# Kernel tuning notes

Hardware: AMD Instinct MI355X
Metric: run time of the kernel (lower is better)

Reference implementation:

```python
import jax, jax.numpy as jnp
import numpy as np

N_NODES = 50000
N_EDGES = 300000
HID = 256


def setup_inputs() -> dict:
    key = jax.random.key(0)
    ks = jax.random.split(key, 8)
    s = lambda fan_in: 1.0 / np.sqrt(fan_in)
    return {
        "node_embeddings": jax.random.normal(ks[0], (N_NODES, HID), dtype=jnp.float32),
        "edge_index": jax.random.randint(ks[1], (2, N_EDGES), 0, N_NODES, dtype=jnp.int64),
        "edge_attr": jax.random.normal(ks[2], (N_EDGES, 3), dtype=jnp.float32),
        "W1": jax.random.normal(ks[3], (2 * HID + 3, HID), dtype=jnp.float32) * s(2 * HID + 3),
        "b1": jnp.zeros((HID,), dtype=jnp.float32),
        "W2": jax.random.normal(ks[4], (HID, HID // 2), dtype=jnp.float32) * s(HID),
        "b2": jnp.zeros((HID // 2,), dtype=jnp.float32),
        "W3": jax.random.normal(ks[5], (HID // 2, HID // 4), dtype=jnp.float32) * s(HID // 2),
        "b3": jnp.zeros((HID // 4,), dtype=jnp.float32),
        "W4": jax.random.normal(ks[6], (HID // 4, 3), dtype=jnp.float32) * s(HID // 4),
        "b4": jnp.zeros((3,), dtype=jnp.float32),
    }


def reference(node_embeddings, edge_index, edge_attr, W1, b1, W2, b2, W3, b3, W4, b4):
    # Gather source/target node embeddings: [E, H] each
    src = node_embeddings[edge_index[0]]
    dst = node_embeddings[edge_index[1]]
    feats = jnp.concatenate([src, dst, edge_attr], axis=-1)  # [E, 2H+3]
    # edge_encoder: Linear -> ReLU -> (Dropout=identity in eval) -> Linear
    h = jax.nn.relu(feats @ W1 + b1)
    h = h @ W2 + b2  # [E, H//2]
    # classifier: Linear -> ReLU -> Linear
    h = jax.nn.relu(h @ W3 + b3)
    logits = h @ W4 + b4  # [E, 3]
    return logits
```

## Files before the change

kernel.cpp:

```cpp
#include <hip/hip_runtime.h>
#include <hip/hip_bf16.h>
#include <stdint.h>
#include <stddef.h>


#define NN 50000
#define NE 300000
#define KG(kq,g2) ((kq)*2+(g2))

using bf16x8 = __attribute__((ext_vector_type(8))) short;
using f32x16 = __attribute__((ext_vector_type(16))) float;
using f32x4  = __attribute__((ext_vector_type(4))) float;
using f32x2  = __attribute__((ext_vector_type(2))) float;
using u32x4  = __attribute__((ext_vector_type(4))) unsigned int;
using u32x2  = __attribute__((ext_vector_type(2))) unsigned int;

#define OFF_PQ   0ULL
#define SZ_PQ    (50000ULL*512ULL*2ULL)
#define OFF_W1   (OFF_PQ + SZ_PQ)
#define SZ_W1    (512ULL*256ULL*2ULL)
#define OFF_W1C  (OFF_W1 + SZ_W1)
#define SZ_W1C   (3ULL*256ULL*4ULL)
#define OFF_W2   (OFF_W1C + SZ_W1C)
#define SZ_W2    (128ULL*256ULL*2ULL)
#define OFF_W3   (OFF_W2 + SZ_W2)
#define SZ_W3    (64ULL*128ULL*2ULL)
#define OFF_W4   (OFF_W3 + SZ_W3)
#define SZ_W4    (16ULL*64ULL*2ULL)
#define OFF_FLAG (OFF_W4 + SZ_W4)
#define WS_NEED  (OFF_FLAG + 16ULL)

__device__ __forceinline__ unsigned short f2bf(float x){
  unsigned u = __float_as_uint(x);
  unsigned r = 0x7FFFu + ((u >> 16) & 1u);
  return (unsigned short)((u + r) >> 16);
}
__device__ __forceinline__ unsigned cvtpk(float lo, float hi){
  unsigned r;
  asm("v_cvt_pk_bf16_f32 %0, %1, %2" : "=v"(r) : "v"(lo), "v"(hi));
  return r;
}
__device__ __forceinline__ f32x2 unpk(unsigned w){
  f32x2 r;
  r[0] = __uint_as_float(w << 16);
  r[1] = __uint_as_float(w & 0xFFFF0000u);
  return r;
}
__device__ __forceinline__ f32x16 mfma32(bf16x8 a, bf16x8 b, f32x16 c){
  return __builtin_amdgcn_mfma_f32_32x32x16_bf16(a, b, c, 0, 0, 0);
}
__device__ __forceinline__ f32x4 mfma16(bf16x8 a, bf16x8 b, f32x4 c){
  return __builtin_amdgcn_mfma_f32_16x16x32_bf16(a, b, c, 0, 0, 0);
}
__device__ __forceinline__ f32x16 zero16(){
  f32x16 v;
#pragma unroll
  for (int i = 0; i < 16; ++i) v[i] = 0.f;
  return v;
}

__global__ void prep_pack(const float* __restrict__ W1, const float* __restrict__ W2,
                          const float* __restrict__ W3, const float* __restrict__ W4,
                          const int* __restrict__ ei32, char* __restrict__ ws)
{
  int i = blockIdx.x * 256 + threadIdx.x;
  unsigned short* w1i = (unsigned short*)(ws + OFF_W1);
  unsigned short* w2i = (unsigned short*)(ws + OFF_W2);
  unsigned short* w3i = (unsigned short*)(ws + OFF_W3);
  unsigned short* w4i = (unsigned short*)(ws + OFF_W4);

  if (i < 131072){
    int j = i & 7, out = (i >> 3) & 511, kg = i >> 12;
    int k = (kg >> 1)*16 + (kg & 1)*8 + j;
    float v = (out < 256) ? W1[(size_t)k*256 + out]
                          : W1[(size_t)(256 + k)*256 + (out - 256)];
    w1i[i] = f2bf(v);
  } else if (i < 131072 + 32768){
    int i2 = i - 131072;
    int j = i2 & 7, out = (i2 >> 3) & 127, sg = i2 >> 10;
    int k = (sg >> 2)*32 + (sg & 3)*8 + j;
    w2i[i2] = f2bf(W2[(size_t)k*128 + out]);
  } else if (i < 131072 + 32768 + 8192){
    int i3 = i - 131072 - 32768;
    int j = i3 & 7, out = (i3 >> 3) & 63, sg = i3 >> 9;
    int k = (sg >> 2)*32 + (sg & 3)*8 + j;
    w3i[i3] = f2bf(W3[(size_t)k*64 + out]);
  } else if (i < 131072 + 32768 + 8192 + 1024){
    int i4 = i - 131072 - 32768 - 8192;
    int j = i4 & 7, out = (i4 >> 3) & 15, sg = i4 >> 7;
    int k = (sg >> 2)*32 + (sg & 3)*8 + j;
    w4i[i4] = (out < 3) ? f2bf(W4[(size_t)k*3 + out]) : (unsigned short)0;
  }
  if (i < 768){
    float* w1c = (float*)(ws + OFF_W1C);
    w1c[i] = W1[(size_t)(512 + i/256)*256 + (i & 255)];
  }
  if (i == 0){
    int f = 1;
    for (int t = 1; t < 64; t += 2) if (ei32[t] != 0) { f = 0; break; }
    *(int*)(ws + OFF_FLAG) = f;
  }
}

__global__ __launch_bounds__(512, 4) void gemm1(const float* __restrict__ emb,
                                                const float* __restrict__ b1,
                                                char* __restrict__ ws)
{
  __shared__ __align__(16) unsigned short embL[32*64*8];

  const int tid = threadIdx.x;
  const int wv = tid >> 6, l = tid & 63, ln = l & 31, g2 = l >> 5;
  const int bid = blockIdx.x;
  const int nb = (bid >> 1) * 64;
  const int oh = bid & 1;
  const int ob = oh*256 + wv*32;
  const unsigned short* w1L = (const unsigned short*)(ws + OFF_W1);
  unsigned short* PQ = (unsigned short*)(ws + OFF_PQ);

  bf16x8 aw[16];
#pragma unroll
  for (int kq = 0; kq < 16; ++kq)
    aw[kq] = *(const bf16x8*)(w1L + ((size_t)KG(kq,g2)*512 + ob + ln)*8);

#pragma unroll
  for (int it = 0; it < 8; ++it){
    int u = it*512 + tid;
    int kg = u >> 7, node = (u >> 1) & 63, half = u & 1;
    int n = nb + node; if (n >= NN) n = NN - 1;
    int k = (kg >> 1)*16 + (kg & 1)*8 + half*4;
    f32x4 e = *(const f32x4*)(emb + (size_t)n*256 + k);
    u32x2 w; w[0] = cvtpk(e[0], e[1]); w[1] = cvtpk(e[2], e[3]);
    *(u32x2*)(embL + (size_t)kg*512 + node*8 + half*4) = w;
  }
  __syncthreads();

  f32x16 acc0 = zero16(), acc1 = zero16();
#pragma unroll
  for (int kq = 0; kq < 16; ++kq){
    bf16x8 b0  = *(const bf16x8*)(embL + ((size_t)KG(kq,g2)*64 +      ln)*8);
    bf16x8 b1v = *(const bf16x8*)(embL + ((size_t)KG(kq,g2)*64 + 32 + ln)*8);
    acc0 = mfma32(aw[kq], b0,  acc0);
    acc1 = mfma32(aw[kq], b1v, acc1);
  }

#pragma unroll
  for (int bg = 0; bg < 2; ++bg){
    int n = nb + bg*32 + ln;
    if (n < NN){
#pragma unroll
      for (int rr = 0; rr < 4; ++rr){
        int o = ob + rr*8 + g2*4;
        f32x4 bv = {0.f,0.f,0.f,0.f};
        if (oh == 0) bv = *(const f32x4*)(b1 + o);
        unsigned d0, d1;
        if (bg == 0){
          d0 = cvtpk(acc0[rr*4+0]+bv[0], acc0[rr*4+1]+bv[1]);
          d1 = cvtpk(acc0[rr*4+2]+bv[2], acc0[rr*4+3]+bv[3]);
        } else {
          d0 = cvtpk(acc1[rr*4+0]+bv[0], acc1[rr*4+1]+bv[1]);
          d1 = cvtpk(acc1[rr*4+2]+bv[2], acc1[rr*4+3]+bv[3]);
        }
        u32x2 st = {d0, d1};
        *(u32x2*)(PQ + (size_t)n*512 + o) = st;
      }
    }
  }
}


#define PAIRX(LO, HI, D) ((D)==0 ? (f32x2){(LO)[0],(LO)[1]} : \
                          (D)==1 ? (f32x2){(LO)[2],(LO)[3]} : \
                          (D)==2 ? (f32x2){(HI)[0],(HI)[1]} : \
                                   (f32x2){(HI)[2],(HI)[3]})

#define L2STEP(S, X)                                                           \
  {                                                                            \
    const int ks_ = (S);                                                       \
    bf16x8 pc = p##X, qc = q##X;                                               \
    int kp = ks_ + 2; if (kp > 7) kp = 7;                                      \
    p##X = *(const bf16x8*)(PQ + (size_t)si*512 + kp*32 + g4*8);               \
    q##X = *(const bf16x8*)(PQ + (size_t)di*512 + 256 + kp*32 + g4*8);         \
    const int kb = ks_*32 + g4*8;                                              \
    f32x4 w0lo = *(const f32x4*)(w1c_lds +   0 + kb);                          \
    f32x4 w0hi = *(const f32x4*)(w1c_lds +   4 + kb);                          \
    f32x4 w1lo = *(const f32x4*)(w1c_lds + 256 + kb);                          \
    f32x4 w1hi = *(const f32x4*)(w1c_lds + 260 + kb);                          \
    f32x4 w2lo = *(const f32x4*)(w1c_lds + 512 + kb);                          \
    f32x4 w2hi = *(const f32x4*)(w1c_lds + 516 + kb);                          \
    u32x4 pu = __builtin_bit_cast(u32x4, pc);                                  \
    u32x4 qu = __builtin_bit_cast(u32x4, qc);                                  \
    f32x2 z2 = {0.f, 0.f};                                                     \
    unsigned bu0, bu1, bu2, bu3;                                               \
    _Pragma("unroll")                                                          \
    for (int d = 0; d < 4; ++d){                                               \
      f32x2 h = unpk(pu[d]) + unpk(qu[d]);                                     \
      h += PAIRX(w0lo, w0hi, d) * at0;                                         \
      h += PAIRX(w1lo, w1hi, d) * at1;                                         \
      h += PAIRX(w2lo, w2hi, d) * at2;                                         \
      h = __builtin_elementwise_max(h, z2);                                    \
      unsigned c = cvtpk(h[0], h[1]);                                          \
      if (d==0) bu0 = c; else if (d==1) bu1 = c; else if (d==2) bu2 = c;       \
      else bu3 = c;                                                            \
    }                                                                          \
    u32x4 buv = {bu0, bu1, bu2, bu3};                                          \
    bf16x8 b = __builtin_bit_cast(bf16x8, buv);                                \
    const char* abase = smem + (size_t)(ks_*4 + g4)*2048 + c16*16;             \
    _Pragma("unroll")                                                          \
    for (int t = 0; t < 8; ++t){                                               \
      bf16x8 af = *(const bf16x8*)(abase + t*256);                             \
      acc2[t] = mfma16(af, b, acc2[t]);                                        \
    }                                                                          \
  }

__global__ __launch_bounds__(512, 4) void fused(const int* __restrict__ eidx,
                                                const float* __restrict__ attr,
                                                const float* __restrict__ b2,
                                                const float* __restrict__ b3,
                                                const float* __restrict__ b4,
                                                const char* __restrict__ ws,
                                                float* __restrict__ out)
{
  __shared__ __align__(16) char smem[68608];
  const int tid = threadIdx.x;
  const int wv = tid >> 6, l = tid & 63, c16 = l & 15, g4 = l >> 4;

  const unsigned short* PQ = (const unsigned short*)(ws + OFF_PQ);
  const float* W1c = (const float*)(ws + OFF_W1C);
  const int flag64 = *(const int*)(ws + OFF_FLAG);
  const float* w1c_lds = (const float*)(smem + 65536);

  {
    const uint4* src = (const uint4*)(ws + OFF_W2);
    uint4* dst = (uint4*)smem;
#pragma unroll
    for (int it = 0; it < 8; ++it) dst[it*512 + tid] = src[it*512 + tid];
    if (tid < 192) ((f32x4*)(smem + 65536))[tid] = ((const f32x4*)W1c)[tid];
  }
  __syncthreads();

  const int eb = blockIdx.x * 128 + wv * 16;
  const int e = eb + c16;
  const bool ev = (e < NE);
  const int ec = ev ? e : 0;
  const int si = flag64 ? eidx[2*(size_t)ec]        : eidx[ec];
  const int di = flag64 ? eidx[2*((size_t)NE + ec)] : eidx[NE + ec];
  const float at0 = ev ? attr[(size_t)ec*3 + 0] : 0.f;
  const float at1 = ev ? attr[(size_t)ec*3 + 1] : 0.f;
  const float at2 = ev ? attr[(size_t)ec*3 + 2] : 0.f;

  f32x4 acc2[8];
#pragma unroll
  for (int t = 0; t < 8; ++t) acc2[t] = (f32x4){0.f,0.f,0.f,0.f};

  bf16x8 pA, qA, pB, qB;
  pA = *(const bf16x8*)(PQ + (size_t)si*512 + g4*8);
  qA = *(const bf16x8*)(PQ + (size_t)di*512 + 256 + g4*8);
  pB = *(const bf16x8*)(PQ + (size_t)si*512 + 32 + g4*8);
  qB = *(const bf16x8*)(PQ + (size_t)di*512 + 256 + 32 + g4*8);

#pragma unroll 1
  for (int sb = 0; sb < 4; ++sb){
    L2STEP(2*sb,     A);
    L2STEP(2*sb + 1, B);
  }

  __syncthreads();

  {
    const uint4* s3 = (const uint4*)(ws + OFF_W3);
    uint4* d3 = (uint4*)(smem + 36864);
    for (int i = tid; i < 1152; i += 512) d3[i] = s3[i];
  }

  unsigned short* hslot = (unsigned short*)(smem + wv*4352);
#pragma unroll
  for (int t = 0; t < 8; ++t){
    f32x4 bv = *(const f32x4*)(b2 + t*16 + g4*4);
    unsigned d0 = cvtpk(acc2[t][0]+bv[0], acc2[t][1]+bv[1]);
    unsigned d1 = cvtpk(acc2[t][2]+bv[2], acc2[t][3]+bv[3]);
    u32x2 st = {d0, d1};
    *(u32x2*)(hslot + (size_t)c16*136 + t*16 + g4*4) = st;
  }
  __syncthreads();

  f32x4 acc3[4];
#pragma unroll
  for (int t = 0; t < 4; ++t) acc3[t] = (f32x4){0.f,0.f,0.f,0.f};
  const char* w3b = smem + 36864;
#pragma unroll
  for (int ks = 0; ks < 4; ++ks){
    bf16x8 bb = *(const bf16x8*)(hslot + (size_t)c16*136 + ks*32 + g4*8);
    const char* ab = w3b + (size_t)(ks*4 + g4)*1024 + c16*16;
#pragma unroll
    for (int t = 0; t < 4; ++t){
      bf16x8 af = *(const bf16x8*)(ab + t*256);
      acc3[t] = mfma16(af, bb, acc3[t]);
    }
  }

#pragma unroll
  for (int t = 0; t < 4; ++t){
    f32x4 bv = *(const f32x4*)(b3 + t*16 + g4*4);
    unsigned d0 = cvtpk(fmaxf(acc3[t][0]+bv[0],0.f), fmaxf(acc3[t][1]+bv[1],0.f));
    unsigned d1 = cvtpk(fmaxf(acc3[t][2]+bv[2],0.f), fmaxf(acc3[t][3]+bv[3],0.f));
    u32x2 st = {d0, d1};
    *(u32x2*)(hslot + (size_t)c16*136 + t*16 + g4*4) = st;
  }

  f32x4 acc4 = {0.f,0.f,0.f,0.f};
  const char* w4b = smem + 53248;
#pragma unroll
  for (int ks = 0; ks < 2; ++ks){
    bf16x8 bb = *(const bf16x8*)(hslot + (size_t)c16*136 + ks*32 + g4*8);
    bf16x8 af = *(const bf16x8*)(w4b + (size_t)(ks*4 + g4)*256 + c16*16);
    acc4 = mfma16(af, bb, acc4);
  }
  if (g4 == 0 && ev){
    out[(size_t)e*3 + 0] = acc4[0] + b4[0];
    out[(size_t)e*3 + 1] = acc4[1] + b4[1];
    out[(size_t)e*3 + 2] = acc4[2] + b4[2];
  }
}

extern "C" void kernel_launch(void* const* d_in, const int* in_sizes, int n_in,
                              void* d_out, int out_size, void* d_ws, size_t ws_size,
                              hipStream_t stream)
{
  const float* emb  = (const float*)d_in[0];
  const int*   eidx = (const int*)  d_in[1];
  const float* attr = (const float*)d_in[2];
  const float* W1   = (const float*)d_in[3];
  const float* b1   = (const float*)d_in[4];
  const float* W2   = (const float*)d_in[5];
  const float* b2   = (const float*)d_in[6];
  const float* W3   = (const float*)d_in[7];
  const float* b3   = (const float*)d_in[8];
  const float* W4   = (const float*)d_in[9];
  const float* b4   = (const float*)d_in[10];
  char* ws = (char*)d_ws;
  float* out = (float*)d_out;

  if (ws_size < WS_NEED) return;

  prep_pack<<<676, 256, 0, stream>>>(W1, W2, W3, W4, eidx, ws);
  gemm1<<<((NN + 63)/64)*2, 512, 0, stream>>>(emb, b1, ws);
  fused<<<(NE + 127)/128, 512, 0, stream>>>(eidx, attr, b2, b3, b4, ws, out);
}
```

Measured before the change: 117.4 us.

## Double per-wave edge and output tiles, deepen PQ gather prefetch with inline asm

gemm1 now has each block compute all 512 outputs for its 64 nodes, so each wave holds two weight tiles and embeddings are loaded and converted once rather than twice. The fused kernel handles 32 edges per wave instead of 16, so each W2 LDS fragment feeds two MFMAs. The PQ gathers are issued three stages ahead with raw global_load asm and explicit vmcnt waits to hide gather latency. W3/W4 are now read straight from global memory instead of being staged in LDS. The cost is higher register pressure, lower launch-bound occupancy (4 to 3 and 2), and fragile hand-managed waitcnt ordering.

After: 148.8 us. 26.8% more time.

```diff
diff --git a/kernel.cpp b/kernel.cpp
--- a/kernel.cpp
+++ b/kernel.cpp
@@ -57,6 +57,9 @@
 #pragma unroll
   for (int i = 0; i < 16; ++i) v[i] = 0.f;
   return v;
+}
+__device__ __forceinline__ void gld16(bf16x8& r, const unsigned short* p){
+  asm volatile("global_load_dwordx4 %0, %1, off" : "=&v"(r) : "v"(p));
 }
 
 __global__ void prep_pack(const float* __restrict__ W1, const float* __restrict__ W2,
@@ -102,7 +105,7 @@
   }
 }
 
-__global__ __launch_bounds__(512, 4) void gemm1(const float* __restrict__ emb,
+__global__ __launch_bounds__(512, 2) void gemm1(const float* __restrict__ emb,
                                                 const float* __restrict__ b1,
                                                 char* __restrict__ ws)
 {
@@ -110,17 +113,18 @@
 
   const int tid = threadIdx.x;
   const int wv = tid >> 6, l = tid & 63, ln = l & 31, g2 = l >> 5;
-  const int bid = blockIdx.x;
-  const int nb = (bid >> 1) * 64;
-  const int oh = bid & 1;
-  const int ob = oh*256 + wv*32;
+  const int nb = blockIdx.x * 64;
+  const int ob = wv * 64;
   const unsigned short* w1L = (const unsigned short*)(ws + OFF_W1);
   unsigned short* PQ = (unsigned short*)(ws + OFF_PQ);
 
-  bf16x8 aw[16];
-#pragma unroll
-  for (int kq = 0; kq < 16; ++kq)
-    aw[kq] = *(const bf16x8*)(w1L + ((size_t)KG(kq,g2)*512 + ob + ln)*8);
+  bf16x8 aw[2][16];
+#pragma unroll
+  for (int kq = 0; kq < 16; ++kq){
+#pragma unroll
+    for (int t2 = 0; t2 < 2; ++t2)
+      aw[t2][kq] = *(const bf16x8*)(w1L + ((size_t)KG(kq,g2)*512 + ob + t2*32 + ln)*8);
+  }
 
 #pragma unroll
   for (int it = 0; it < 8; ++it){
@@ -134,34 +138,35 @@
   }
   __syncthreads();
 
-  f32x16 acc0 = zero16(), acc1 = zero16();
+  f32x16 acc[2][2];
+  acc[0][0] = zero16(); acc[0][1] = zero16();
+  acc[1][0] = zero16(); acc[1][1] = zero16();
 #pragma unroll
   for (int kq = 0; kq < 16; ++kq){
     bf16x8 b0  = *(const bf16x8*)(embL + ((size_t)KG(kq,g2)*64 +      ln)*8);
     bf16x8 b1v = *(const bf16x8*)(embL + ((size_t)KG(kq,g2)*64 + 32 + ln)*8);
-    acc0 = mfma32(aw[kq], b0,  acc0);
-    acc1 = mfma32(aw[kq], b1v, acc1);
-  }
-
-#pragma unroll
-  for (int bg = 0; bg < 2; ++bg){
-    int n = nb + bg*32 + ln;
-    if (n < NN){
-#pragma unroll
-      for (int rr = 0; rr < 4; ++rr){
-        int o = ob + rr*8 + g2*4;
-        f32x4 bv = {0.f,0.f,0.f,0.f};
-        if (oh == 0) bv = *(const f32x4*)(b1 + o);
-        unsigned d0, d1;
-        if (bg == 0){
-          d0 = cvtpk(acc0[rr*4+0]+bv[0], acc0[rr*4+1]+bv[1]);
-          d1 = cvtpk(acc0[rr*4+2]+bv[2], acc0[rr*4+3]+bv[3]);
-        } else {
-          d0 = cvtpk(acc1[rr*4+0]+bv[0], acc1[rr*4+1]+bv[1]);
-          d1 = cvtpk(acc1[rr*4+2]+bv[2], acc1[rr*4+3]+bv[3]);
+    acc[0][0] = mfma32(aw[0][kq], b0,  acc[0][0]);
+    acc[1][0] = mfma32(aw[1][kq], b0,  acc[1][0]);
+    acc[0][1] = mfma32(aw[0][kq], b1v, acc[0][1]);
+    acc[1][1] = mfma32(aw[1][kq], b1v, acc[1][1]);
+  }
+
+#pragma unroll
+  for (int t2 = 0; t2 < 2; ++t2){
+#pragma unroll
+    for (int bg = 0; bg < 2; ++bg){
+      int n = nb + bg*32 + ln;
+      if (n < NN){
+#pragma unroll
+        for (int rr = 0; rr < 4; ++rr){
+          int o = ob + t2*32 + rr*8 + g2*4;
+          f32x4 bv = {0.f,0.f,0.f,0.f};
+          if (ob + t2*32 < 256) bv = *(const f32x4*)(b1 + o);
+          unsigned d0 = cvtpk(acc[t2][bg][rr*4+0]+bv[0], acc[t2][bg][rr*4+1]+bv[1]);
+          unsigned d1 = cvtpk(acc[t2][bg][rr*4+2]+bv[2], acc[t2][bg][rr*4+3]+bv[3]);
+          u32x2 st = {d0, d1};
+          *(u32x2*)(PQ + (size_t)n*512 + o) = st;
         }
-        u32x2 st = {d0, d1};
-        *(u32x2*)(PQ + (size_t)n*512 + o) = st;
       }
     }
   }
@@ -173,46 +178,58 @@
                           (D)==2 ? (f32x2){(HI)[0],(HI)[1]} : \
                                    (f32x2){(HI)[2],(HI)[3]})
 
-#define L2STEP(S, X)                                                           \
+#define H1BUILD(PC, QC, A0, A1, A2, BOUT)                                      \
   {                                                                            \
-    const int ks_ = (S);                                                       \
-    bf16x8 pc = p##X, qc = q##X;                                               \
-    int kp = ks_ + 2; if (kp > 7) kp = 7;                                      \
-    p##X = *(const bf16x8*)(PQ + (size_t)si*512 + kp*32 + g4*8);               \
-    q##X = *(const bf16x8*)(PQ + (size_t)di*512 + 256 + kp*32 + g4*8);         \
-    const int kb = ks_*32 + g4*8;                                              \
+    u32x4 pu = __builtin_bit_cast(u32x4, PC);                                  \
+    u32x4 qu = __builtin_bit_cast(u32x4, QC);                                  \
+    f32x2 z2 = {0.f, 0.f};                                                     \
+    unsigned bu0, bu1, bu2, bu3;                                               \
+    _Pragma("unroll")                                                          \
+    for (int d = 0; d < 4; ++d){                                               \
+      f32x2 h = unpk(pu[d]) + unpk(qu[d]);                                     \
+      h += PAIRX(w0lo, w0hi, d) * (A0);                                        \
+      h += PAIRX(w1lo, w1hi, d) * (A1);                                        \
+      h += PAIRX(w2lo, w2hi, d) * (A2);                                        \
+      h = __builtin_elementwise_max(h, z2);                                    \
+      unsigned c = cvtpk(h[0], h[1]);                                          \
+      if (d==0) bu0 = c; else if (d==1) bu1 = c; else if (d==2) bu2 = c;       \
+      else bu3 = c;                                                            \
+    }                                                                          \
+    u32x4 buv = {bu0, bu1, bu2, bu3};                                          \
+    BOUT = __builtin_bit_cast(bf16x8, buv);                                    \
+  }
+
+#define PQWAIT(N, P0, Q0, P1, Q1) \
+  asm volatile("s_waitcnt vmcnt(" #N ")" : "+v"(P0), "+v"(Q0), "+v"(P1), "+v"(Q1))
+
+#define ISSUE4(P0, Q0, P1, Q1, S)                                              \
+  { gld16(P0, Prow0 + (S)*32); gld16(Q0, Qrow0 + (S)*32);                      \
+    gld16(P1, Prow1 + (S)*32); gld16(Q1, Qrow1 + (S)*32); }
+
+#define L2S(S, VM, P0, Q0, P1, Q1, DO_ISS, IS)                                 \
+  {                                                                            \
+    PQWAIT(VM, P0, Q0, P1, Q1);                                                \
+    const int kb = (S)*32 + g4*8;                                              \
     f32x4 w0lo = *(const f32x4*)(w1c_lds +   0 + kb);                          \
     f32x4 w0hi = *(const f32x4*)(w1c_lds +   4 + kb);                          \
     f32x4 w1lo = *(const f32x4*)(w1c_lds + 256 + kb);                          \
     f32x4 w1hi = *(const f32x4*)(w1c_lds + 260 + kb);                          \
     f32x4 w2lo = *(const f32x4*)(w1c_lds + 512 + kb);                          \
     f32x4 w2hi = *(const f32x4*)(w1c_lds + 516 + kb);                          \
-    u32x4 pu = __builtin_bit_cast(u32x4, pc);                                  \
-    u32x4 qu = __builtin_bit_cast(u32x4, qc);                                  \
-    f32x2 z2 = {0.f, 0.f};                                                     \
-    unsigned bu0, bu1, bu2, bu3;                                               \
-    _Pragma("unroll")                                                          \
-    for (int d = 0; d < 4; ++d){                                               \
-      f32x2 h = unpk(pu[d]) + unpk(qu[d]);                                     \
-      h += PAIRX(w0lo, w0hi, d) * at0;                                         \
-      h += PAIRX(w1lo, w1hi, d) * at1;                                         \
-      h += PAIRX(w2lo, w2hi, d) * at2;                                         \
-      h = __builtin_elementwise_max(h, z2);                                    \
-      unsigned c = cvtpk(h[0], h[1]);                                          \
-      if (d==0) bu0 = c; else if (d==1) bu1 = c; else if (d==2) bu2 = c;       \
-      else bu3 = c;                                                            \
-    }                                                                          \
-    u32x4 buv = {bu0, bu1, bu2, bu3};                                          \
-    bf16x8 b = __builtin_bit_cast(bf16x8, buv);                                \
-    const char* abase = smem + (size_t)(ks_*4 + g4)*2048 + c16*16;             \
+    bf16x8 b0, b1;                                                             \
+    H1BUILD(P0, Q0, at0e0, at1e0, at2e0, b0);                                  \
+    H1BUILD(P1, Q1, at0e1, at1e1, at2e1, b1);                                  \
+    if (DO_ISS) { ISSUE4(P0, Q0, P1, Q1, IS); }                                \
+    const char* abase = smem + (size_t)((S)*4 + g4)*2048 + c16*16;             \
     _Pragma("unroll")                                                          \
     for (int t = 0; t < 8; ++t){                                               \
       bf16x8 af = *(const bf16x8*)(abase + t*256);                             \
-      acc2[t] = mfma16(af, b, acc2[t]);                                        \
+      acc2[t][0] = mfma16(af, b0, acc2[t][0]);                                 \
+      acc2[t][1] = mfma16(af, b1, acc2[t][1]);                                 \
     }                                                                          \
   }
 
-__global__ __launch_bounds__(512, 4) void fused(const int* __restrict__ eidx,
+__global__ __launch_bounds__(512, 3) void fused(const int* __restrict__ eidx,
                                                 const float* __restrict__ attr,
                                                 const float* __restrict__ b2,
                                                 const float* __restrict__ b3,
@@ -220,15 +237,45 @@
                                                 const char* __restrict__ ws,
                                                 float* __restrict__ out)
 {
-  __shared__ __align__(16) char smem[68608];
+  __shared__ __align__(16) char smem[65536 + 3072];
   const int tid = threadIdx.x;
   const int wv = tid >> 6, l = tid & 63, c16 = l & 15, g4 = l >> 4;
 
-  const unsigned short* PQ = (const unsigned short*)(ws + OFF_PQ);
+  const unsigned short* PQ  = (const unsigned short*)(ws + OFF_PQ);
+  const unsigned short* w3g = (const unsigned short*)(ws + OFF_W3);
+  const unsigned short* w4g = (const unsigned short*)(ws + OFF_W4);
   const float* W1c = (const float*)(ws + OFF_W1C);
   const int flag64 = *(const int*)(ws + OFF_FLAG);
   const float* w1c_lds = (const float*)(smem + 65536);
 
+  const int ebase = blockIdx.x * 256 + wv * 32;
+  const int e0 = ebase + c16,      e1 = ebase + 16 + c16;
+  const bool ev0 = (e0 < NE),      ev1 = (e1 < NE);
+  const int ec0 = ev0 ? e0 : 0,    ec1 = ev1 ? e1 : 0;
+  const int si0 = flag64 ? eidx[2*(size_t)ec0]        : eidx[ec0];
+  const int di0 = flag64 ? eidx[2*((size_t)NE + ec0)] : eidx[NE + ec0];
+  const int si1 = flag64 ? eidx[2*(size_t)ec1]        : eidx[ec1];
+  const int di1 = flag64 ? eidx[2*((size_t)NE + ec1)] : eidx[NE + ec1];
+
+  float at0e0 = ev0 ? attr[(size_t)ec0*3 + 0] : 0.f;
+  float at1e0 = ev0 ? attr[(size_t)ec0*3 + 1] : 0.f;
+  float at2e0 = ev0 ? attr[(size_t)ec0*3 + 2] : 0.f;
+  float at0e1 = ev1 ? attr[(size_t)ec1*3 + 0] : 0.f;
+  float at1e1 = ev1 ? attr[(size_t)ec1*3 + 1] : 0.f;
+  float at2e1 = ev1 ? attr[(size_t)ec1*3 + 2] : 0.f;
+  asm volatile("" : "+v"(at0e0), "+v"(at1e0), "+v"(at2e0),
+                    "+v"(at0e1), "+v"(at1e1), "+v"(at2e1));
+
+  const unsigned short* Prow0 = PQ + (size_t)si0*512 + g4*8;
+  const unsigned short* Qrow0 = PQ + (size_t)di0*512 + 256 + g4*8;
+  const unsigned short* Prow1 = PQ + (size_t)si1*512 + g4*8;
+  const unsigned short* Qrow1 = PQ + (size_t)di1*512 + 256 + g4*8;
+
+  bf16x8 pA0, qA0, pA1, qA1, pB0, qB0, pB1, qB1, pC0, qC0, pC1, qC1;
+  ISSUE4(pA0, qA0, pA1, qA1, 0);
+  ISSUE4(pB0, qB0, pB1, qB1, 1);
+  ISSUE4(pC0, qC0, pC1, qC1, 2);
+
   {
     const uint4* src = (const uint4*)(ws + OFF_W2);
     uint4* dst = (uint4*)smem;
@@ -238,87 +285,89 @@
   }
   __syncthreads();
 
-  const int eb = blockIdx.x * 128 + wv * 16;
-  const int e = eb + c16;
-  const bool ev = (e < NE);
-  const int ec = ev ? e : 0;
-  const int si = flag64 ? eidx[2*(size_t)ec]        : eidx[ec];
-  const int di = flag64 ? eidx[2*((size_t)NE + ec)] : eidx[NE + ec];
-  const float at0 = ev ? attr[(size_t)ec*3 + 0] : 0.f;
-  const float at1 = ev ? attr[(size_t)ec*3 + 1] : 0.f;
-  const float at2 = ev ? attr[(size_t)ec*3 + 2] : 0.f;
-
-  f32x4 acc2[8];
-#pragma unroll
-  for (int t = 0; t < 8; ++t) acc2[t] = (f32x4){0.f,0.f,0.f,0.f};
-
-  bf16x8 pA, qA, pB, qB;
-  pA = *(const bf16x8*)(PQ + (size_t)si*512 + g4*8);
-  qA = *(const bf16x8*)(PQ + (size_t)di*512 + 256 + g4*8);
-  pB = *(const bf16x8*)(PQ + (size_t)si*512 + 32 + g4*8);
-  qB = *(const bf16x8*)(PQ + (size_t)di*512 + 256 + 32 + g4*8);
-
-#pragma unroll 1
-  for (int sb = 0; sb < 4; ++sb){
-    L2STEP(2*sb,     A);
-    L2STEP(2*sb + 1, B);
-  }
+  f32x4 acc2[8][2];
+#pragma unroll
+  for (int t = 0; t < 8; ++t){ acc2[t][0] = (f32x4){0,0,0,0}; acc2[t][1] = (f32x4){0,0,0,0}; }
+
+  L2S(0, 8, pA0, qA0, pA1, qA1, 1, 3);
+  L2S(1, 8, pB0, qB0, pB1, qB1, 1, 4);
+  L2S(2, 8, pC0, qC0, pC1, qC1, 1, 5);
+  L2S(3, 8, pA0, qA0, pA1, qA1, 1, 6);
+  L2S(4, 8, pB0, qB0, pB1, qB1, 1, 7);
+  L2S(5, 8, pC0, qC0, pC1, qC1, 0, 0);
+  L2S(6, 4, pA0, qA0, pA1, qA1, 0, 0);
+  L2S(7, 0, pB0, qB0, pB1, qB1, 0, 0);
 
   __syncthreads();
 
-  {
-    const uint4* s3 = (const uint4*)(ws + OFF_W3);
-    uint4* d3 = (uint4*)(smem + 36864);
-    for (int i = tid; i < 1152; i += 512) d3[i] = s3[i];
-  }
-
-  unsigned short* hslot = (unsigned short*)(smem + wv*4352);
+  unsigned short* hslot = (unsigned short*)(smem + wv*8192);
 #pragma unroll
   for (int t = 0; t < 8; ++t){
     f32x4 bv = *(const f32x4*)(b2 + t*16 + g4*4);
-    unsigned d0 = cvtpk(acc2[t][0]+bv[0], acc2[t][1]+bv[1]);
-    unsigned d1 = cvtpk(acc2[t][2]+bv[2], acc2[t][3]+bv[3]);
-    u32x2 st = {d0, d1};
-    *(u32x2*)(hslot + (size_t)c16*136 + t*16 + g4*4) = st;
-  }
-  __syncthreads();
-
-  f32x4 acc3[4];
-#pragma unroll
-  for (int t = 0; t < 4; ++t) acc3[t] = (f32x4){0.f,0.f,0.f,0.f};
-  const char* w3b = smem + 36864;
+    const int sg_o = t*2 + (g4 >> 1);
+    const int j0 = (g4 & 1)*4;
+#pragma unroll
+    for (int g = 0; g < 2; ++g){
+      unsigned d0 = cvtpk(acc2[t][g][0]+bv[0], acc2[t][g][1]+bv[1]);
+      unsigned d1 = cvtpk(acc2[t][g][2]+bv[2], acc2[t][g][3]+bv[3]);
+      u32x2 st = {d0, d1};
+      *(u32x2*)(hslot + ((sg_o*32 + g*16 + c16)*8 + j0)) = st;
+    }
+  }
+
+  f32x4 acc3[4][2];
+#pragma unroll
+  for (int t = 0; t < 4; ++t){ acc3[t][0] = (f32x4){0,0,0,0}; acc3[t][1] = (f32x4){0,0,0,0}; }
 #pragma unroll
   for (int ks = 0; ks < 4; ++ks){
-    bf16x8 bb = *(const bf16x8*)(hslot + (size_t)c16*136 + ks*32 + g4*8);
-    const char* ab = w3b + (size_t)(ks*4 + g4)*1024 + c16*16;
+    const int sg = ks*4 + g4;
+    bf16x8 bb0 = *(const bf16x8*)(hslot + (sg*32 +      c16)*8);
+    bf16x8 bb1 = *(const bf16x8*)(hslot + (sg*32 + 16 + c16)*8);
 #pragma unroll
     for (int t = 0; t < 4; ++t){
-      bf16x8 af = *(const bf16x8*)(ab + t*256);
-      acc3[t] = mfma16(af, bb, acc3[t]);
+      bf16x8 af = *(const bf16x8*)(w3g + ((size_t)sg*64 + t*16 + c16)*8);
+      acc3[t][0] = mfma16(af, bb0, acc3[t][0]);
+      acc3[t][1] = mfma16(af, bb1, acc3[t][1]);
     }
   }
 
 #pragma unroll
   for (int t = 0; t < 4; ++t){
     f32x4 bv = *(const f32x4*)(b3 + t*16 + g4*4);
-    unsigned d0 = cvtpk(fmaxf(acc3[t][0]+bv[0],0.f), fmaxf(acc3[t][1]+bv[1],0.f));
-    unsigned d1 = cvtpk(fmaxf(acc3[t][2]+bv[2],0.f), fmaxf(acc3[t][3]+bv[3],0.f));
-    u32x2 st = {d0, d1};
-    *(u32x2*)(hslot + (size_t)c16*136 + t*16 + g4*4) = st;
-  }
-
-  f32x4 acc4 = {0.f,0.f,0.f,0.f};
-  const char* w4b = smem + 53248;
+    const int sg_o = t*2 + (g4 >> 1);
+    const int j0 = (g4 & 1)*4;
+#pragma unroll
+    for (int g = 0; g < 2; ++g){
+      unsigned d0 = cvtpk(fmaxf(acc3[t][g][0]+bv[0],0.f), fmaxf(acc3[t][g][1]+bv[1],0.f));
+      unsigned d1 = cvtpk(fmaxf(acc3[t][g][2]+bv[2],0.f), fmaxf(acc3[t][g][3]+bv[3],0.f));
+      u32x2 st = {d0, d1};
+      *(u32x2*)(hslot + ((sg_o*32 + g*16 + c16)*8 + j0)) = st;
+    }
+  }
+
+  f32x4 acc4[2];
+  acc4[0] = (f32x4){0,0,0,0}; acc4[1] = (f32x4){0,0,0,0};
 #pragma unroll
   for (int ks = 0; ks < 2; ++ks){
-    bf16x8 bb = *(const bf16x8*)(hslot + (size_t)c16*136 + ks*32 + g4*8);
-    bf16x8 af = *(const bf16x8*)(w4b + (size_t)(ks*4 + g4)*256 + c16*16);
-    acc4 = mfma16(af, bb, acc4);
-  }
-  if (g4 == 0 && ev){
-    out[(size_t)e*3 + 0] = acc4[0] + b4[0];
-    out[(size_t)e*3 + 1] = acc4[1] + b4[1];
-    out[(size_t)e*3 + 2] = acc4[2] + b4[2];
+    const int sg = ks*4 + g4;
+    bf16x8 af = *(const bf16x8*)(w4g + ((size_t)sg*16 + c16)*8);
+    bf16x8 bb0 = *(const bf16x8*)(hslot + (sg*32 +      c16)*8);
+    bf16x8 bb1 = *(const bf16x8*)(hslot + (sg*32 + 16 + c16)*8);
+    acc4[0] = mfma16(af, bb0, acc4[0]);
+    acc4[1] = mfma16(af, bb1, acc4[1]);
+  }
+  if (g4 == 0){
+    float c0 = b4[0], c1 = b4[1], c2 = b4[2];
+    if (ev0){
+      out[(size_t)e0*3 + 0] = acc4[0][0] + c0;
+      out[(size_t)e0*3 + 1] = acc4[0][1] + c1;
+      out[(size_t)e0*3 + 2] = acc4[0][2] + c2;
+    }
+    if (ev1){
+      out[(size_t)e1*3 + 0] = acc4[1][0] + c0;
+      out[(size_t)e1*3 + 1] = acc4[1][1] + c1;
+      out[(size_t)e1*3 + 2] = acc4[1][2] + c2;
+    }
   }
 }
 
@@ -343,6 +392,6 @@
   if (ws_size < WS_NEED) return;
 
   prep_pack<<<676, 256, 0, stream>>>(W1, W2, W3, W4, eidx, ws);
-  gemm1<<<((NN + 63)/64)*2, 512, 0, stream>>>(emb, b1, ws);
-  fused<<<(NE + 127)/128, 512, 0, stream>>>(eidx, attr, b2, b3, b4, ws, out);
-}
+  gemm1<<<(NN + 63)/64, 512, 0, stream>>>(emb, b1, ws);
+  fused<<<(NE + 255)/256, 512, 0, stream>>>(eidx, attr, b2, b3, b4, ws, out);
+}
```
